# Kernel optimization log

Measured on AMD Instinct MI355X. Metric: run time of the kernel, lower is better.

The kernel has to match this reference:

```python
import jax, jax.numpy as jnp
import numpy as np

B, S, D, H = 2, 2048, 1024, 16
DK = D // H
ALPHA = 0.5


def setup_inputs() -> dict:
    key = jax.random.key(0)
    ks = jax.random.split(key, 16)
    scale = 0.02
    return {
        "q": jax.random.normal(ks[0], (B, S, D), dtype=jnp.float32),
        "k": jax.random.normal(ks[1], (B, S, D), dtype=jnp.float32),
        "v": jax.random.normal(ks[2], (B, S, D), dtype=jnp.float32),
        "attn_mask": jax.random.randint(ks[3], (S, S), 0, 2, dtype=jnp.int32),
        "causal_mask": jax.random.uniform(ks[4], (S, S), dtype=jnp.float32),
        "Wq": jax.random.normal(ks[5], (D, D), dtype=jnp.float32) * scale,
        "bq": jnp.zeros((D,), dtype=jnp.float32),
        "Wk": jax.random.normal(ks[6], (D, D), dtype=jnp.float32) * scale,
        "bk": jnp.zeros((D,), dtype=jnp.float32),
        "Wv": jax.random.normal(ks[7], (D, D), dtype=jnp.float32) * scale,
        "bv": jnp.zeros((D,), dtype=jnp.float32),
        "Wo": jax.random.normal(ks[8], (D, D), dtype=jnp.float32) * scale,
        "bo": jnp.zeros((D,), dtype=jnp.float32),
    }


def _split_heads(x):
    # [B, S, D] -> [B, H, S, DK]
    return x.reshape(B, S, H, DK).transpose(0, 2, 1, 3)


def reference(q, k, v, attn_mask, causal_mask, Wq, bq, Wk, bk, Wv, bv, Wo, bo):
    qh = _split_heads(q @ Wq.T + bq)
    kh = _split_heads(k @ Wk.T + bk)
    vh = _split_heads(v @ Wv.T + bv)
    scores = jnp.einsum("bhqd,bhkd->bhqk", qh, kh) / jnp.sqrt(jnp.float32(DK))
    # additive mask: positions where attn_mask == 1 get -1e9 (broadcast [S,S] -> [B,H,S,S])
    scores = jnp.where(attn_mask[None, None] == 1, jnp.float32(-1e9), scores)
    # multiplicative causal scaling (applied AFTER the fill, as in the original)
    scores = scores * (1.0 + ALPHA * causal_mask[None, None])
    probs = jax.nn.softmax(scores, axis=-1)  # dropout is identity in eval / p=0
    attn = jnp.einsum("bhqk,bhkd->bhqd", probs, vh)  # [B, H, S, DK]
    concat = attn.transpose(0, 2, 1, 3).reshape(B, S, D)
    out = concat @ Wo.T + bo
    return (out, attn)
```

## Files before the change

### kernel.cpp

```cpp
#include <hip/hip_runtime.h>
#include <hip/hip_bf16.h>

#define NB 2
#define NS 2048
#define ND 1024
#define NH 16
#define NDK 64
#define GK 1024

using bf16_t = __hip_bfloat16;
typedef __attribute__((ext_vector_type(8))) short bf16x8;
typedef __attribute__((ext_vector_type(4))) float f32x4;
typedef unsigned short u16;
typedef unsigned int u32;

#define SC_LOG2E 0.1803368801f

static __device__ __forceinline__ u16 f2bf(float f) {
    __hip_bfloat16 h = __float2bfloat16(f);
    return *reinterpret_cast<u16*>(&h);
}

#define GLDS16(gp, lp)                                                                    \
    __builtin_amdgcn_global_load_lds((const __attribute__((address_space(1))) void*)(gp), \
                                     (__attribute__((address_space(3))) void*)(lp), 16, 0, 0)

struct CvtArgs {
    const float* s[4];
    u16* d[4];
};

__global__ void f2b_multi(CvtArgs a) {
    const float* s = a.s[blockIdx.y];
    u16* d = a.d[blockIdx.y];
    int i = blockIdx.x * 256 + threadIdx.x;
    float4 v = reinterpret_cast<const float4*>(s)[i];
    ushort4 o;
    o.x = f2bf(v.x);
    o.y = f2bf(v.y);
    o.z = f2bf(v.z);
    o.w = f2bf(v.w);
    reinterpret_cast<ushort4*>(d)[i] = o;
}

__global__ void mask_combine_kernel(const int* __restrict__ am,
                                    const float* __restrict__ cm,
                                    float* __restrict__ outc) {
    int i = (blockIdx.x * 256 + threadIdx.x) * 4;
    int4 a = *reinterpret_cast<const int4*>(am + i);
    float4 c = *reinterpret_cast<const float4*>(cm + i);
    float4 r;
    r.x = (a.x == 1) ? -1.0f : fmaf(0.5f * SC_LOG2E, c.x, SC_LOG2E);
    r.y = (a.y == 1) ? -1.0f : fmaf(0.5f * SC_LOG2E, c.y, SC_LOG2E);
    r.z = (a.z == 1) ? -1.0f : fmaf(0.5f * SC_LOG2E, c.z, SC_LOG2E);
    r.w = (a.w == 1) ? -1.0f : fmaf(0.5f * SC_LOG2E, c.w, SC_LOG2E);
    *reinterpret_cast<float4*>(outc + i) = r;
}

struct MMArgs {
    const u16* A;
    const u16* W;
    const float* bias;
    void* out;
};

template <int BN, int MODE>
__global__ __launch_bounds__(256) void mm_glds(MMArgs g0, MMArgs g1, MMArgs g2) {
    const MMArgs ga = (blockIdx.z == 0) ? g0 : (blockIdx.z == 1) ? g1 : g2;
    constexpr int BM = 128, BK = 32;
    constexpr int JN = BN / 32;
    __shared__ __align__(16) u16 As[2][BM * BK];
    __shared__ __align__(16) u16 Bs[2][BN * BK];

    const int tid = threadIdx.x;
    const int lane = tid & 63;
    const int w = tid >> 6;
    const int wm = w >> 1, wn = w & 1;
    const int fr = lane & 15, fg = lane >> 4;
    const int bm0 = blockIdx.y * BM, bn0 = blockIdx.x * BN;

    const u16* agp = ga.A + (size_t)(bm0 + w * 32 + (lane >> 2)) * GK + (lane & 3) * 8;
    const u16* bgp = ga.W +
                     (size_t)(bn0 + w * (BN == 128 ? 32 : 16) + (lane >> 2)) * GK +
                     (lane & 3) * 8;

    f32x4 acc[4][JN];
    const f32x4 z4 = {0.f, 0.f, 0.f, 0.f};
#pragma unroll
    for (int i = 0; i < 4; ++i)
#pragma unroll
        for (int j = 0; j < JN; ++j) acc[i][j] = z4;

    {
        u16* la = &As[0][w * 1024];
        u16* lb = &Bs[0][w * (BN == 128 ? 1024 : 512)];
        GLDS16(agp, la);
        GLDS16(agp + 16 * GK, la + 512);
        if (BN == 128) {
            GLDS16(bgp, lb);
            GLDS16(bgp + 16 * GK, lb + 512);
        } else {
            GLDS16(bgp, lb);
        }
    }
    __syncthreads();

    int cur = 0;
    for (int kt = 0; kt < GK / BK; ++kt) {
        if (kt + 1 < GK / BK) {
            const int ko = (kt + 1) * BK;
            u16* la = &As[cur ^ 1][w * 1024];
            u16* lb = &Bs[cur ^ 1][w * (BN == 128 ? 1024 : 512)];
            GLDS16(agp + ko, la);
            GLDS16(agp + ko + 16 * GK, la + 512);
            if (BN == 128) {
                GLDS16(bgp + ko, lb);
                GLDS16(bgp + ko + 16 * GK, lb + 512);
            } else {
                GLDS16(bgp + ko, lb);
            }
        }
        bf16x8 af[4], bfr[JN];
#pragma unroll
        for (int i = 0; i < 4; ++i)
            af[i] = *(const bf16x8*)&As[cur][(wm * 64 + i * 16 + fr) * BK + fg * 8];
#pragma unroll
        for (int j = 0; j < JN; ++j)
            bfr[j] = *(const bf16x8*)&Bs[cur][(wn * (BN / 2) + j * 16 + fr) * BK + fg * 8];
#pragma unroll
        for (int i = 0; i < 4; ++i)
#pragma unroll
            for (int j = 0; j < JN; ++j)
                acc[i][j] = __builtin_amdgcn_mfma_f32_16x16x32_bf16(af[i], bfr[j], acc[i][j],
                                                                    0, 0, 0);
        __syncthreads();
        cur ^= 1;
    }

#pragma unroll
    for (int j = 0; j < JN; ++j) {
        const int col = bn0 + wn * (BN / 2) + j * 16 + fr;
        const float bv_ = ga.bias[col];
#pragma unroll
        for (int i = 0; i < 4; ++i) {
#pragma unroll
            for (int r = 0; r < 4; ++r) {
                const int row = bm0 + wm * 64 + i * 16 + fg * 4 + r;
                const float val = acc[i][j][r] + bv_;
                if (MODE == 1) {
                    const int b_ = row >> 11, s_ = row & (NS - 1);
                    const int h_ = col >> 6, dk = col & (NDK - 1);
                    ((bf16_t*)ga.out)[(((size_t)(b_ * NH + h_)) * NS + s_) * NDK + dk] =
                        __float2bfloat16(val);
                } else {
                    ((float*)ga.out)[(size_t)row * ND + col] = val;
                }
            }
        }
    }
}

__global__ __launch_bounds__(256) void vtrans_kernel(const u16* __restrict__ Vh,
                                                     u16* __restrict__ VhT) {
    __shared__ __align__(16) u16 T[64][72];
    const int t = threadIdx.x;
    const int bh = blockIdx.y;
    const int s0 = blockIdx.x * 64;
    const size_t boff = (size_t)bh * NS * NDK;

    const int vkp = t & 31;
    const int vdk = (t >> 5) * 8;
    int4 va = *(const int4*)(Vh + boff + (size_t)(s0 + 2 * vkp) * NDK + vdk);
    int4 vb = *(const int4*)(Vh + boff + (size_t)(s0 + 2 * vkp + 1) * NDK + vdk);
    {
        const u16* a = (const u16*)&va;
        const u16* b = (const u16*)&vb;
#pragma unroll
        for (int j = 0; j < 8; ++j) {
            u32 pk = (u32)a[j] | ((u32)b[j] << 16);
            *(u32*)&T[vdk + j][2 * vkp] = pk;
        }
    }
    __syncthreads();
    const int d = t >> 2;
    const int so = (t & 3) * 16;
    int4 o0 = *(const int4*)&T[d][so];
    int4 o1 = *(const int4*)&T[d][so + 8];
    u16* op = VhT + boff + (size_t)d * NS + s0 + so;
    *(int4*)(op) = o0;
    *(int4*)(op + 8) = o1;
}

__global__ __launch_bounds__(256) void flash_mfma(const u16* __restrict__ Qh,
                                                  const u16* __restrict__ Kh,
                                                  const u16* __restrict__ VhT,
                                                  const float* __restrict__ comb,
                                                  float* __restrict__ attnOut,
                                                  u16* __restrict__ concatOut) {
    __shared__ __align__(16) u16 Kt[2][64 * 64];
    __shared__ __align__(16) u16 Vt[2][64 * 64];
    __shared__ __align__(16) u16 Pt[4][16][64];

    const int tid = threadIdx.x;
    const int w = tid >> 6;
    const int lane = tid & 63;
    const int qc = lane & 15;
    const int g = lane >> 4;
    const int bh = blockIdx.y;
    const int b_ = bh >> 4, h_ = bh & 15;
    const int qw = blockIdx.x * 64 + w * 16;

    const size_t bhoff = (size_t)bh * NS * NDK;

    const int srow = lane >> 3;
    const int sblk = (lane & 7) ^ srow;
    const u16* kgp = Kh + bhoff + (size_t)(w * 16 + srow) * NDK + sblk * 8;
    const u16* vgp = VhT + bhoff + (size_t)(w * 16 + srow) * NS + sblk * 8;

    bf16x8 qf[2];
    {
        const u16* qp = Qh + bhoff + (size_t)(qw + qc) * NDK + g * 8;
        qf[0] = *(const bf16x8*)(qp);
        qf[1] = *(const bf16x8*)(qp + 32);
    }

    const f32x4 z4 = {0.f, 0.f, 0.f, 0.f};
    f32x4 o[4];
    o[0] = o[1] = o[2] = o[3] = z4;
    float lsum = 0.f;

    const float* crow = comb + (size_t)(qw + qc) * NS;
    const int kxor = qc & 7;
    const int pxor = (qc & 7) << 4;
    char* ptrow = (char*)&Pt[w][0][0] + qc * 128;

    {
        u16* kd = &Kt[0][(w * 16) * 64];
        u16* vd = &Vt[0][(w * 16) * 64];
        GLDS16(kgp, kd);
        GLDS16(kgp + 8 * NDK, kd + 512);
        GLDS16(vgp, vd);
        GLDS16(vgp + 8 * NS, vd + 512);
    }
    __syncthreads();

    int cur = 0;
    for (int kt = 0; kt < NS; kt += 64) {
        if (kt + 64 < NS) {
            u16* kd = &Kt[cur ^ 1][(w * 16) * 64];
            u16* vd = &Vt[cur ^ 1][(w * 16) * 64];
            GLDS16(kgp + (kt + 64) * NDK, kd);
            GLDS16(kgp + (kt + 64 + 8) * NDK, kd + 512);
            GLDS16(vgp + (kt + 64), vd);
            GLDS16(vgp + 8 * NS + (kt + 64), vd + 512);
        }

        f32x4 s[4];
        s[0] = s[1] = s[2] = s[3] = z4;
#pragma unroll
        for (int kc = 0; kc < 2; ++kc) {
#pragma unroll
            for (int ks = 0; ks < 4; ++ks) {
                bf16x8 kf = *(const bf16x8*)&Kt[cur][(ks * 16 + qc) * 64 +
                                                     (((kc << 2) | g) ^ kxor) * 8];
                s[ks] = __builtin_amdgcn_mfma_f32_16x16x32_bf16(kf, qf[kc], s[ks], 0, 0, 0);
            }
        }

#pragma unroll
        for (int ks = 0; ks < 4; ++ks) {
            float4 c4 = *(const float4*)(crow + kt + ks * 16 + g * 4);
            const float* cc = (const float*)&c4;
            float p0 = exp2f(s[ks][0] * cc[0]);
            float p1 = exp2f(s[ks][1] * cc[1]);
            float p2 = exp2f(s[ks][2] * cc[2]);
            float p3 = exp2f(s[ks][3] * cc[3]);
            p0 = (cc[0] < 0.f) ? 0.f : p0;
            p1 = (cc[1] < 0.f) ? 0.f : p1;
            p2 = (cc[2] < 0.f) ? 0.f : p2;
            p3 = (cc[3] < 0.f) ? 0.f : p3;
            lsum += (p0 + p1) + (p2 + p3);
            uint2 pw;
            pw.x = (u32)f2bf(p0) | ((u32)f2bf(p1) << 16);
            pw.y = (u32)f2bf(p2) | ((u32)f2bf(p3) << 16);
            *(uint2*)(ptrow + ((ks * 32 + g * 8) ^ pxor)) = pw;
        }

#pragma unroll
        for (int kc = 0; kc < 2; ++kc) {
            bf16x8 pf = *(const bf16x8*)(ptrow + ((kc * 64 + g * 16) ^ pxor));
#pragma unroll
            for (int dsub = 0; dsub < 4; ++dsub) {
                bf16x8 vf = *(const bf16x8*)&Vt[cur][(dsub * 16 + qc) * 64 +
                                                     (((kc << 2) | g) ^ kxor) * 8];
                o[dsub] = __builtin_amdgcn_mfma_f32_16x16x32_bf16(pf, vf, o[dsub], 0, 0, 0);
            }
        }
        __syncthreads();
        cur ^= 1;
    }

    lsum += __shfl_xor(lsum, 16);
    lsum += __shfl_xor(lsum, 32);
    const float linv = 1.0f / lsum;
    float inv[4];
#pragma unroll
    for (int r = 0; r < 4; ++r) inv[r] = __shfl(linv, g * 4 + r);

#pragma unroll
    for (int dsub = 0; dsub < 4; ++dsub) {
#pragma unroll
        for (int r = 0; r < 4; ++r) {
            const float val = o[dsub][r] * inv[r];
            const int qg = qw + g * 4 + r;
            const int d = dsub * 16 + qc;
            attnOut[bhoff + (size_t)qg * NDK + d] = val;
            concatOut[((size_t)b_ * NS + qg) * ND + h_ * NDK + d] = f2bf(val);
        }
    }
}

extern "C" void kernel_launch(void* const* d_in, const int* in_sizes, int n_in,
                              void* d_out, int out_size, void* d_ws, size_t ws_size,
                              hipStream_t stream) {
    const float* q = (const float*)d_in[0];
    const float* k = (const float*)d_in[1];
    const float* v = (const float*)d_in[2];
    const int* am = (const int*)d_in[3];
    const float* cm = (const float*)d_in[4];
    const float* Wq = (const float*)d_in[5];
    const float* bq = (const float*)d_in[6];
    const float* Wk = (const float*)d_in[7];
    const float* bk = (const float*)d_in[8];
    const float* Wv = (const float*)d_in[9];
    const float* bv = (const float*)d_in[10];
    const float* Wo = (const float*)d_in[11];
    const float* bo = (const float*)d_in[12];

    float* out = (float*)d_out;
    float* attn_out = out + (size_t)NB * NS * ND;

    char* p = (char*)d_ws;
    float* CB = (float*)p;  p += (size_t)NS * NS * 4;
    u16* qb = (u16*)p;      p += (size_t)NB * NS * ND * 2;
    u16* kb_ = (u16*)p;     p += (size_t)NB * NS * ND * 2;
    u16* vb_ = (u16*)p;     p += (size_t)NB * NS * ND * 2;
    u16* Wqb = (u16*)p;     p += (size_t)ND * ND * 2;
    u16* Wkb = (u16*)p;     p += (size_t)ND * ND * 2;
    u16* Wvb = (u16*)p;     p += (size_t)ND * ND * 2;
    u16* Wob = (u16*)p;     p += (size_t)ND * ND * 2;
    u16* Qh = (u16*)p;      p += (size_t)NB * NS * ND * 2;
    u16* Kh = (u16*)p;      p += (size_t)NB * NS * ND * 2;
    u16* Vh = (u16*)p;      p += (size_t)NB * NS * ND * 2;
    u16* VhT = (u16*)p;     p += (size_t)NB * NS * ND * 2;
    u16* CCb = (u16*)p;     p += (size_t)NB * NS * ND * 2;

    const int n4_in = NB * NS * ND / 4;
    const int n4_w = ND * ND / 4;

    hipLaunchKernelGGL(mask_combine_kernel, dim3(4096), dim3(256), 0, stream, am, cm, CB);

    CvtArgs ci;
    ci.s[0] = q;  ci.d[0] = qb;
    ci.s[1] = k;  ci.d[1] = kb_;
    ci.s[2] = v;  ci.d[2] = vb_;
    ci.s[3] = q;  ci.d[3] = qb;
    hipLaunchKernelGGL(f2b_multi, dim3(n4_in / 256, 3), dim3(256), 0, stream, ci);

    CvtArgs cw;
    cw.s[0] = Wq; cw.d[0] = Wqb;
    cw.s[1] = Wk; cw.d[1] = Wkb;
    cw.s[2] = Wv; cw.d[2] = Wvb;
    cw.s[3] = Wo; cw.d[3] = Wob;
    hipLaunchKernelGGL(f2b_multi, dim3(n4_w / 256, 4), dim3(256), 0, stream, cw);

    MMArgs mq = {qb, Wqb, bq, (void*)Qh};
    MMArgs mk = {kb_, Wkb, bk, (void*)Kh};
    MMArgs mv = {vb_, Wvb, bv, (void*)Vh};
    hipLaunchKernelGGL((mm_glds<128, 1>), dim3(ND / 128, 4096 / 128, 3), dim3(256), 0, stream,
                       mq, mk, mv);

    hipLaunchKernelGGL(vtrans_kernel, dim3(NS / 64, NB * NH), dim3(256), 0, stream, Vh, VhT);

    hipLaunchKernelGGL(flash_mfma, dim3(NS / 64, NB * NH), dim3(256), 0, stream, Qh, Kh, VhT,
                       CB, attn_out, CCb);

    MMArgs mo = {CCb, Wob, bo, (void*)out};
    hipLaunchKernelGGL((mm_glds<64, 0>), dim3(ND / 64, 4096 / 128, 1), dim3(256), 0, stream,
                       mo, mo, mo);
}
```

Measured before the change: 191.7 us.

## Tune flash attention inner loop and fuse the preprocessing launches

Merges the mask-combine and the two fp32-to-bf16 conversion kernels into one prep launch. In the flash kernel, the mask/scale row for the next tile is prefetched into registers one iteration ahead. The row sum now comes from an extra MFMA against a ones vector instead of scalar adds and shuffles. The loop also uses the hardware exp2 intrinsic and the packed v_cvt_pk_bf16_f32 conversion, raises wave priority around the MFMA blocks, and unrolls by 2. These changes aim to cut launch overhead, hide global load latency and trim VALU work. The cost is extra register pressure and a denominator computed from bf16-rounded probabilities.

Result: slower. 195.7 us (+2.1%).

```diff
diff --git a/kernel.cpp b/kernel.cpp
--- a/kernel.cpp
+++ b/kernel.cpp
@@ -21,40 +21,52 @@
     return *reinterpret_cast<u16*>(&h);
 }
 
+static __device__ __forceinline__ u32 cvtpk2(float a, float b) {
+    u32 r;
+    asm("v_cvt_pk_bf16_f32 %0, %1, %2" : "=v"(r) : "v"(a), "v"(b));
+    return r;
+}
+
 #define GLDS16(gp, lp)                                                                    \
     __builtin_amdgcn_global_load_lds((const __attribute__((address_space(1))) void*)(gp), \
                                      (__attribute__((address_space(3))) void*)(lp), 16, 0, 0)
 
-struct CvtArgs {
-    const float* s[4];
-    u16* d[4];
+struct PrepArgs {
+    const float* qkv_s[3];
+    u16* qkv_d[3];
+    const float* w_s[4];
+    u16* w_d[4];
+    const int* am;
+    const float* cm;
+    float* comb;
 };
 
-__global__ void f2b_multi(CvtArgs a) {
-    const float* s = a.s[blockIdx.y];
-    u16* d = a.d[blockIdx.y];
-    int i = blockIdx.x * 256 + threadIdx.x;
-    float4 v = reinterpret_cast<const float4*>(s)[i];
-    ushort4 o;
-    o.x = f2bf(v.x);
-    o.y = f2bf(v.y);
-    o.z = f2bf(v.z);
-    o.w = f2bf(v.w);
-    reinterpret_cast<ushort4*>(d)[i] = o;
-}
-
-__global__ void mask_combine_kernel(const int* __restrict__ am,
-                                    const float* __restrict__ cm,
-                                    float* __restrict__ outc) {
-    int i = (blockIdx.x * 256 + threadIdx.x) * 4;
-    int4 a = *reinterpret_cast<const int4*>(am + i);
-    float4 c = *reinterpret_cast<const float4*>(cm + i);
-    float4 r;
-    r.x = (a.x == 1) ? -1.0f : fmaf(0.5f * SC_LOG2E, c.x, SC_LOG2E);
-    r.y = (a.y == 1) ? -1.0f : fmaf(0.5f * SC_LOG2E, c.y, SC_LOG2E);
-    r.z = (a.z == 1) ? -1.0f : fmaf(0.5f * SC_LOG2E, c.z, SC_LOG2E);
-    r.w = (a.w == 1) ? -1.0f : fmaf(0.5f * SC_LOG2E, c.w, SC_LOG2E);
-    *reinterpret_cast<float4*>(outc + i) = r;
+__global__ __launch_bounds__(256) void prep_kernel(PrepArgs a) {
+    const int x = blockIdx.x, y = blockIdx.y, tid = threadIdx.x;
+    if (y < 3) {
+        int i = x * 256 + tid;
+        float4 v = reinterpret_cast<const float4*>(a.qkv_s[y])[i];
+        ushort4 o;
+        o.x = f2bf(v.x); o.y = f2bf(v.y); o.z = f2bf(v.z); o.w = f2bf(v.w);
+        reinterpret_cast<ushort4*>(a.qkv_d[y])[i] = o;
+    } else if (y == 3) {
+        int w = x >> 10;
+        int i = (x & 1023) * 256 + tid;
+        float4 v = reinterpret_cast<const float4*>(a.w_s[w])[i];
+        ushort4 o;
+        o.x = f2bf(v.x); o.y = f2bf(v.y); o.z = f2bf(v.z); o.w = f2bf(v.w);
+        reinterpret_cast<ushort4*>(a.w_d[w])[i] = o;
+    } else {
+        int i = (x * 256 + tid) * 4;
+        int4 m = *reinterpret_cast<const int4*>(a.am + i);
+        float4 c = *reinterpret_cast<const float4*>(a.cm + i);
+        float4 r;
+        r.x = (m.x == 1) ? -1.0f : fmaf(0.5f * SC_LOG2E, c.x, SC_LOG2E);
+        r.y = (m.y == 1) ? -1.0f : fmaf(0.5f * SC_LOG2E, c.y, SC_LOG2E);
+        r.z = (m.z == 1) ? -1.0f : fmaf(0.5f * SC_LOG2E, c.z, SC_LOG2E);
+        r.w = (m.w == 1) ? -1.0f : fmaf(0.5f * SC_LOG2E, c.w, SC_LOG2E);
+        *reinterpret_cast<float4*>(a.comb + i) = r;
+    }
 }
 
 struct MMArgs {
@@ -224,10 +236,14 @@
         qf[1] = *(const bf16x8*)(qp + 32);
     }
 
+    bf16x8 vones;
+#pragma unroll
+    for (int j = 0; j < 8; ++j) vones[j] = (short)0x3F80;
+
     const f32x4 z4 = {0.f, 0.f, 0.f, 0.f};
     f32x4 o[4];
     o[0] = o[1] = o[2] = o[3] = z4;
-    float lsum = 0.f;
+    f32x4 o_l = z4;
 
     const float* crow = comb + (size_t)(qw + qc) * NS;
     const int kxor = qc & 7;
@@ -242,9 +258,14 @@
         GLDS16(vgp, vd);
         GLDS16(vgp + 8 * NS, vd + 512);
     }
+    float4 cpre[4];
+#pragma unroll
+    for (int ks = 0; ks < 4; ++ks)
+        cpre[ks] = *(const float4*)(crow + ks * 16 + g * 4);
     __syncthreads();
 
     int cur = 0;
+#pragma unroll 2
     for (int kt = 0; kt < NS; kt += 64) {
         if (kt + 64 < NS) {
             u16* kd = &Kt[cur ^ 1][(w * 16) * 64];
@@ -254,9 +275,18 @@
             GLDS16(vgp + (kt + 64), vd);
             GLDS16(vgp + 8 * NS + (kt + 64), vd + 512);
         }
+        float4 cc4[4];
+#pragma unroll
+        for (int ks = 0; ks < 4; ++ks) cc4[ks] = cpre[ks];
+        if (kt + 64 < NS) {
+#pragma unroll
+            for (int ks = 0; ks < 4; ++ks)
+                cpre[ks] = *(const float4*)(crow + kt + 64 + ks * 16 + g * 4);
+        }
 
         f32x4 s[4];
         s[0] = s[1] = s[2] = s[3] = z4;
+        __builtin_amdgcn_s_setprio(1);
 #pragma unroll
         for (int kc = 0; kc < 2; ++kc) {
 #pragma unroll
@@ -266,29 +296,30 @@
                 s[ks] = __builtin_amdgcn_mfma_f32_16x16x32_bf16(kf, qf[kc], s[ks], 0, 0, 0);
             }
         }
+        __builtin_amdgcn_s_setprio(0);
 
 #pragma unroll
         for (int ks = 0; ks < 4; ++ks) {
-            float4 c4 = *(const float4*)(crow + kt + ks * 16 + g * 4);
-            const float* cc = (const float*)&c4;
-            float p0 = exp2f(s[ks][0] * cc[0]);
-            float p1 = exp2f(s[ks][1] * cc[1]);
-            float p2 = exp2f(s[ks][2] * cc[2]);
-            float p3 = exp2f(s[ks][3] * cc[3]);
+            const float* cc = (const float*)&cc4[ks];
+            float p0 = __builtin_amdgcn_exp2f(s[ks][0] * cc[0]);
+            float p1 = __builtin_amdgcn_exp2f(s[ks][1] * cc[1]);
+            float p2 = __builtin_amdgcn_exp2f(s[ks][2] * cc[2]);
+            float p3 = __builtin_amdgcn_exp2f(s[ks][3] * cc[3]);
             p0 = (cc[0] < 0.f) ? 0.f : p0;
             p1 = (cc[1] < 0.f) ? 0.f : p1;
             p2 = (cc[2] < 0.f) ? 0.f : p2;
             p3 = (cc[3] < 0.f) ? 0.f : p3;
-            lsum += (p0 + p1) + (p2 + p3);
             uint2 pw;
-            pw.x = (u32)f2bf(p0) | ((u32)f2bf(p1) << 16);
-            pw.y = (u32)f2bf(p2) | ((u32)f2bf(p3) << 16);
+            pw.x = cvtpk2(p0, p1);
+            pw.y = cvtpk2(p2, p3);
             *(uint2*)(ptrow + ((ks * 32 + g * 8) ^ pxor)) = pw;
         }
 
+        __builtin_amdgcn_s_setprio(1);
 #pragma unroll
         for (int kc = 0; kc < 2; ++kc) {
             bf16x8 pf = *(const bf16x8*)(ptrow + ((kc * 64 + g * 16) ^ pxor));
+            o_l = __builtin_amdgcn_mfma_f32_16x16x32_bf16(pf, vones, o_l, 0, 0, 0);
 #pragma unroll
             for (int dsub = 0; dsub < 4; ++dsub) {
                 bf16x8 vf = *(const bf16x8*)&Vt[cur][(dsub * 16 + qc) * 64 +
@@ -296,16 +327,14 @@
                 o[dsub] = __builtin_amdgcn_mfma_f32_16x16x32_bf16(pf, vf, o[dsub], 0, 0, 0);
             }
         }
+        __builtin_amdgcn_s_setprio(0);
         __syncthreads();
         cur ^= 1;
     }
 
-    lsum += __shfl_xor(lsum, 16);
-    lsum += __shfl_xor(lsum, 32);
-    const float linv = 1.0f / lsum;
     float inv[4];
 #pragma unroll
-    for (int r = 0; r < 4; ++r) inv[r] = __shfl(linv, g * 4 + r);
+    for (int r = 0; r < 4; ++r) inv[r] = 1.0f / o_l[r];
 
 #pragma unroll
     for (int dsub = 0; dsub < 4; ++dsub) {
@@ -355,24 +384,18 @@
     u16* VhT = (u16*)p;     p += (size_t)NB * NS * ND * 2;
     u16* CCb = (u16*)p;     p += (size_t)NB * NS * ND * 2;
 
-    const int n4_in = NB * NS * ND / 4;
-    const int n4_w = ND * ND / 4;
-
-    hipLaunchKernelGGL(mask_combine_kernel, dim3(4096), dim3(256), 0, stream, am, cm, CB);
-
-    CvtArgs ci;
-    ci.s[0] = q;  ci.d[0] = qb;
-    ci.s[1] = k;  ci.d[1] = kb_;
-    ci.s[2] = v;  ci.d[2] = vb_;
-    ci.s[3] = q;  ci.d[3] = qb;
-    hipLaunchKernelGGL(f2b_multi, dim3(n4_in / 256, 3), dim3(256), 0, stream, ci);
-
-    CvtArgs cw;
-    cw.s[0] = Wq; cw.d[0] = Wqb;
-    cw.s[1] = Wk; cw.d[1] = Wkb;
-    cw.s[2] = Wv; cw.d[2] = Wvb;
-    cw.s[3] = Wo; cw.d[3] = Wob;
-    hipLaunchKernelGGL(f2b_multi, dim3(n4_w / 256, 4), dim3(256), 0, stream, cw);
+    PrepArgs pa;
+    pa.qkv_s[0] = q;  pa.qkv_d[0] = qb;
+    pa.qkv_s[1] = k;  pa.qkv_d[1] = kb_;
+    pa.qkv_s[2] = v;  pa.qkv_d[2] = vb_;
+    pa.w_s[0] = Wq;   pa.w_d[0] = Wqb;
+    pa.w_s[1] = Wk;   pa.w_d[1] = Wkb;
+    pa.w_s[2] = Wv;   pa.w_d[2] = Wvb;
+    pa.w_s[3] = Wo;   pa.w_d[3] = Wob;
+    pa.am = am;
+    pa.cm = cm;
+    pa.comb = CB;
+    hipLaunchKernelGGL(prep_kernel, dim3(4096, 5), dim3(256), 0, stream, pa);
 
     MMArgs mq = {qb, Wqb, bq, (void*)Qh};
     MMArgs mk = {kb_, Wkb, bk, (void*)Kh};
```
